# Performance work log

Hardware: AMD Instinct MI355X
Metric: run time of the kernel (lower is better)

The kernel has to match this reference:

```python
import jax, jax.numpy as jnp
import numpy as np

N, E, F_IN, HEADS, OUT_PER_HEAD = 50000, 1600000, 128, 4, 32
NEG_SLOPE = 0.2  # LeakyReLU slope used by standard GATConv


def setup_inputs() -> dict:
    key = jax.random.key(0)
    ks = jax.random.split(key, 7)
    x = jax.random.normal(ks[0], (N, F_IN), dtype=jnp.float32)
    edge_src = jax.random.randint(ks[1], (E,), 0, N, dtype=jnp.int64)
    edge_dst = jax.random.randint(ks[2], (E,), 0, N, dtype=jnp.int64)
    W = jax.random.normal(ks[3], (F_IN, HEADS * OUT_PER_HEAD), dtype=jnp.float32) / np.float32(np.sqrt(F_IN))
    a_src = jax.random.normal(ks[4], (HEADS, OUT_PER_HEAD), dtype=jnp.float32) * 0.1
    a_dst = jax.random.normal(ks[5], (HEADS, OUT_PER_HEAD), dtype=jnp.float32) * 0.1
    bias = jnp.zeros((HEADS * OUT_PER_HEAD,), dtype=jnp.float32)
    return {"x": x, "W": W, "a_src": a_src, "a_dst": a_dst, "bias": bias,
            "edge_src": edge_src, "edge_dst": edge_dst}


def reference(x, W, a_src, a_dst, bias, edge_src, edge_dst):
    # GATConv with concat=True over a static edge list (the faithful
    # static-shape form of tf.where(adj>0.5) -> gather -> GAT -> scatter).
    n = x.shape[0]
    H, D = a_src.shape
    h = (x @ W).reshape(n, H, D)                      # [N,H,D] projected features
    # per-node attention logits for source / destination roles
    e_s = jnp.einsum('nhd,hd->nh', h, a_src)          # [N,H]
    e_d = jnp.einsum('nhd,hd->nh', h, a_dst)          # [N,H]
    # per-edge logits with LeakyReLU
    e = jax.nn.leaky_relu(e_s[edge_src] + e_d[edge_dst], NEG_SLOPE)  # [E,H]
    # numerically stable softmax over incoming edges of each destination node
    m = jax.ops.segment_max(e, edge_dst, num_segments=n)             # [N,H]
    m = jnp.where(jnp.isfinite(m), m, 0.0)
    alpha = jnp.exp(e - m[edge_dst])                                 # [E,H]
    denom = jax.ops.segment_sum(alpha, edge_dst, num_segments=n)     # [N,H]
    alpha = alpha / jnp.where(denom > 0, denom, 1.0)[edge_dst]
    # weighted aggregation of source features onto destinations
    msgs = alpha[:, :, None] * h[edge_src]                           # [E,H,D]
    out = jax.ops.segment_sum(msgs, edge_dst, num_segments=n)        # [N,H,D]
    return out.reshape(n, H * D) + bias
```

## Files before the change

### kernel.cpp

```cpp
#include <hip/hip_runtime.h>
#include <math.h>

#define NEG_SLOPE 0.2f
#define XROW 136
#define BSHIFT 4
#define BNODES 16
#define NBUCK_MAX 3200
#define CAP 768
#define CPAD 32
#define NSB 256
#define STASH 6272

typedef __attribute__((ext_vector_type(8))) short short8;
typedef __attribute__((ext_vector_type(4))) float floatx4;

__device__ __forceinline__ unsigned short f2bf(float f) {
    unsigned int u = __float_as_uint(f);
    u += 0x7fffu + ((u >> 16) & 1u);
    return (unsigned short)(u >> 16);
}
__device__ __forceinline__ float bf2f(unsigned short b) {
    return __uint_as_float(((unsigned int)b) << 16);
}
__device__ __forceinline__ float u2fl(unsigned int u) {
    return __uint_as_float(u << 16);
}
__device__ __forceinline__ float u2fh(unsigned int u) {
    return __uint_as_float(u & 0xffff0000u);
}

__device__ __forceinline__ void fma8(float* a, int o, float wt, const uint4& hv) {
    a[o + 0] = fmaf(wt, u2fl(hv.x), a[o + 0]);
    a[o + 1] = fmaf(wt, u2fh(hv.x), a[o + 1]);
    a[o + 2] = fmaf(wt, u2fl(hv.y), a[o + 2]);
    a[o + 3] = fmaf(wt, u2fh(hv.y), a[o + 3]);
    a[o + 4] = fmaf(wt, u2fl(hv.z), a[o + 4]);
    a[o + 5] = fmaf(wt, u2fh(hv.z), a[o + 5]);
    a[o + 6] = fmaf(wt, u2fl(hv.w), a[o + 6]);
    a[o + 7] = fmaf(wt, u2fh(hv.w), a[o + 7]);
}

__global__ __launch_bounds__(256) void prep_w_kernel(
    const float* __restrict__ W, unsigned short* __restrict__ WThi,
    unsigned short* __restrict__ WTlo, int* __restrict__ gcur, int nbuck)
{
    const int idx = blockIdx.x * 256 + threadIdx.x;
    const int j = idx >> 7, k = idx & 127;
    const float w = W[k * 128 + j];
    const unsigned short hi = f2bf(w);
    WThi[idx] = hi;
    WTlo[idx] = f2bf(w - bf2f(hi));
    if (idx < nbuck) gcur[idx * CPAD] = idx * CAP;
}

__global__ __launch_bounds__(1024) void scatter_kernel(
    const int* __restrict__ src, const int* __restrict__ dst,
    int* __restrict__ gcur, int* __restrict__ ebuf, int e, int nbuck)
{
    __shared__ unsigned int stash[STASH];
    __shared__ int cnt[NBUCK_MAX];
    const int t = threadIdx.x;
    for (int b = t; b < nbuck; b += 1024) cnt[b] = 0;
    __syncthreads();
    const int eph = (((e + NSB - 1) / NSB) + 3) & ~3;
    const int base = blockIdx.x * eph;
    const int m = min(e - base, eph);
    if (m > 0) {
        const int m4 = m >> 2;
        for (int j = t; j < m4; j += 1024) {
            const int i0 = base + j * 4;
            const int4 s4 = *(const int4*)(src + i0);
            const int4 d4 = *(const int4*)(dst + i0);
            stash[j * 4 + 0] = (unsigned)s4.x | ((unsigned)(d4.x & 15) << 16)
                             | ((unsigned)(d4.x >> BSHIFT) << 20);
            atomicAdd(&cnt[d4.x >> BSHIFT], 1);
            stash[j * 4 + 1] = (unsigned)s4.y | ((unsigned)(d4.y & 15) << 16)
                             | ((unsigned)(d4.y >> BSHIFT) << 20);
            atomicAdd(&cnt[d4.y >> BSHIFT], 1);
            stash[j * 4 + 2] = (unsigned)s4.z | ((unsigned)(d4.z & 15) << 16)
                             | ((unsigned)(d4.z >> BSHIFT) << 20);
            atomicAdd(&cnt[d4.z >> BSHIFT], 1);
            stash[j * 4 + 3] = (unsigned)s4.w | ((unsigned)(d4.w & 15) << 16)
                             | ((unsigned)(d4.w >> BSHIFT) << 20);
            atomicAdd(&cnt[d4.w >> BSHIFT], 1);
        }
        for (int j = m4 * 4 + t; j < m; j += 1024) {
            const int d = dst[base + j];
            stash[j] = (unsigned)src[base + j] | ((unsigned)(d & 15) << 16)
                     | ((unsigned)(d >> BSHIFT) << 20);
            atomicAdd(&cnt[d >> BSHIFT], 1);
        }
    }
    __syncthreads();
    for (int b = t; b < nbuck; b += 1024) {
        const int c = cnt[b];
        if (c > 0) cnt[b] = atomicAdd(&gcur[b * CPAD], c);
    }
    __syncthreads();
    for (int j = t; j < m; j += 1024) {
        const unsigned int v = stash[j];
        const int bk = v >> 20;
        const int pos = atomicAdd(&cnt[bk], 1);
        if (pos < bk * CAP + CAP) ebuf[pos] = (int)(v & 0xFFFFFu);
    }
}

__global__ __launch_bounds__(256, 2) void mfma_gemm_kernel(
    const float* __restrict__ x, const unsigned short* __restrict__ WThi,
    const unsigned short* __restrict__ WTlo, const float* __restrict__ a_src,
    const float* __restrict__ a_dst, unsigned short* __restrict__ hb,
    float* __restrict__ es, float* __restrict__ ed, int n)
{
    __shared__ unsigned short Xhi[32 * XROW];
    __shared__ unsigned short Xlo[32 * XROW];
    const int t = threadIdx.x;
    const int wv = t >> 6, lane = t & 63;
    const int l16 = lane & 15, quad = lane >> 4;
    const int node_base = blockIdx.x * 32;

    float4 xv[4];
    #pragma unroll
    for (int it = 0; it < 4; ++it) {
        const int i = t + it * 256;
        const int nd = i >> 5, k4 = i & 31;
        float4 v = make_float4(0.f, 0.f, 0.f, 0.f);
        if (node_base + nd < n)
            v = ((const float4*)(x + (size_t)(node_base + nd) * 128))[k4];
        xv[it] = v;
    }
    #pragma unroll
    for (int it = 0; it < 4; ++it) {
        const int i = t + it * 256;
        const int nd = i >> 5, k4 = i & 31;
        const float4 v = xv[it];
        const unsigned short h0 = f2bf(v.x), h1 = f2bf(v.y),
                             h2 = f2bf(v.z), h3 = f2bf(v.w);
        const unsigned short l0 = f2bf(v.x - bf2f(h0)), l1 = f2bf(v.y - bf2f(h1)),
                             l2 = f2bf(v.z - bf2f(h2)), l3 = f2bf(v.w - bf2f(h3));
        *(ushort4*)&Xhi[nd * XROW + k4 * 4] = make_ushort4(h0, h1, h2, h3);
        *(ushort4*)&Xlo[nd * XROW + k4 * 4] = make_ushort4(l0, l1, l2, l3);
    }

    short8 bh[4][2], bl[4][2];
    #pragma unroll
    for (int c = 0; c < 4; ++c) {
        #pragma unroll
        for (int u = 0; u < 2; ++u) {
            const int j = (wv * 2 + u) * 16 + l16;
            const int ko = c * 32 + quad * 8;
            bh[c][u] = *(const short8*)&WThi[j * 128 + ko];
            bl[c][u] = *(const short8*)&WTlo[j * 128 + ko];
        }
    }
    __syncthreads();

    floatx4 acc[2][2] = {};
    #pragma unroll
    for (int c = 0; c < 4; ++c) {
        const int ko = c * 32 + quad * 8;
        short8 ah[2], al[2];
        #pragma unroll
        for (int r = 0; r < 2; ++r) {
            ah[r] = *(const short8*)&Xhi[(r * 16 + l16) * XROW + ko];
            al[r] = *(const short8*)&Xlo[(r * 16 + l16) * XROW + ko];
        }
        #pragma unroll
        for (int r = 0; r < 2; ++r)
        #pragma unroll
        for (int u = 0; u < 2; ++u) {
            acc[r][u] = __builtin_amdgcn_mfma_f32_16x16x32_bf16(ah[r], bl[c][u], acc[r][u], 0, 0, 0);
            acc[r][u] = __builtin_amdgcn_mfma_f32_16x16x32_bf16(al[r], bh[c][u], acc[r][u], 0, 0, 0);
            acc[r][u] = __builtin_amdgcn_mfma_f32_16x16x32_bf16(ah[r], bh[c][u], acc[r][u], 0, 0, 0);
        }
    }

    float asv[2], adv[2];
    #pragma unroll
    for (int u = 0; u < 2; ++u) {
        const int feat = (wv * 2 + u) * 16 + l16;
        asv[u] = a_src[feat];
        adv[u] = a_dst[feat];
    }
    #pragma unroll
    for (int r = 0; r < 2; ++r) {
        #pragma unroll
        for (int u = 0; u < 2; ++u) {
            const int feat = (wv * 2 + u) * 16 + l16;
            #pragma unroll
            for (int g = 0; g < 4; ++g) {
                const int node = node_base + r * 16 + quad * 4 + g;
                if (node < n)
                    hb[(size_t)node * 128 + feat] = f2bf(acc[r][u][g]);
            }
        }
        #pragma unroll
        for (int g = 0; g < 4; ++g) {
            float ps = acc[r][0][g] * asv[0] + acc[r][1][g] * asv[1];
            float pd = acc[r][0][g] * adv[0] + acc[r][1][g] * adv[1];
            #pragma unroll
            for (int o = 8; o >= 1; o >>= 1) {
                ps += __shfl_xor(ps, o);
                pd += __shfl_xor(pd, o);
            }
            const int node = node_base + r * 16 + quad * 4 + g;
            if (l16 == 0 && node < n) {
                es[node * 4 + wv] = ps;
                ed[node * 4 + wv] = pd;
            }
        }
    }
}

__global__ __launch_bounds__(256) void sort_agg_kernel(
    const unsigned short* __restrict__ hb, const float* __restrict__ es,
    const float* __restrict__ ed, const float* __restrict__ bias,
    const int* __restrict__ gcur, const int* __restrict__ ebuf,
    float* __restrict__ out, int n)
{
    __shared__ unsigned short esort[CAP];
    __shared__ int hist[BNODES], hexcl[BNODES], cur[BNODES];
    const int b = blockIdx.x;
    const int t = threadIdx.x;
    const int lane = t & 63;
    const int wv = t >> 6;
    const int l8 = lane & 7;
    const int oct = lane >> 3;
    const int f0 = l8 * 16;
    const int hh = l8 >> 1;

    const int start = b * CAP;
    const int end = start + min(gcur[b * CPAD] - start, CAP);

    if (t < BNODES) hist[t] = 0;
    __syncthreads();
    for (int i = start + t; i < end; i += 256)
        atomicAdd(&hist[(ebuf[i] >> 16) & (BNODES - 1)], 1);
    __syncthreads();
    if (wv == 0) {
        const int v = (lane < BNODES) ? hist[lane] : 0;
        int incl = v;
        #pragma unroll
        for (int o = 1; o < BNODES; o <<= 1) {
            const int tt = __shfl_up(incl, o);
            if (lane >= o) incl += tt;
        }
        if (lane < BNODES) { hexcl[lane] = incl - v; cur[lane] = incl - v; }
    }
    __syncthreads();
    for (int i = start + t; i < end; i += 256) {
        const int v = ebuf[i];
        const int pos = atomicAdd(&cur[(v >> 16) & (BNODES - 1)], 1);
        if (pos < CAP) esort[pos] = (unsigned short)(v & 0xFFFF);
    }
    __syncthreads();

    for (int j = 0; j < 4; ++j) {
        const int nd = wv * 4 + j;
        const int node = b * BNODES + nd;
        if (node >= n) break;
        const int off = hexcl[nd];
        const int deg = hist[nd];
        const float edh = ed[(size_t)node * 4 + hh];

        float a[16];
        #pragma unroll
        for (int k = 0; k < 16; ++k) a[k] = 0.f;
        float wsum = 0.f;

        for (int c0 = 0; c0 < deg; c0 += 16) {
            const int ci0 = c0 + oct;
            const int ci1 = ci0 + 8;
            const int dm = deg - 1;
            const int s0 = esort[min(off + min(ci0, dm), CAP - 1)];
            const int s1 = esort[min(off + min(ci1, dm), CAP - 1)];
            const float e0 = es[(size_t)s0 * 4 + hh];
            const float e1 = es[(size_t)s1 * 4 + hh];
            const uint4 hA0 = *(const uint4*)&hb[(size_t)s0 * 128 + f0];
            const uint4 hB0 = *(const uint4*)&hb[(size_t)s0 * 128 + f0 + 8];
            const uint4 hA1 = *(const uint4*)&hb[(size_t)s1 * 128 + f0];
            const uint4 hB1 = *(const uint4*)&hb[(size_t)s1 * 128 + f0 + 8];
            float lg0 = e0 + edh; lg0 = lg0 > 0.f ? lg0 : NEG_SLOPE * lg0;
            float lg1 = e1 + edh; lg1 = lg1 > 0.f ? lg1 : NEG_SLOPE * lg1;
            const float w0 = (ci0 < deg) ? __expf(lg0) : 0.f;
            const float w1 = (ci1 < deg) ? __expf(lg1) : 0.f;
            fma8(a, 0, w0, hA0); fma8(a, 8, w0, hB0);
            fma8(a, 0, w1, hA1); fma8(a, 8, w1, hB1);
            wsum += w0 + w1;
        }
        #pragma unroll
        for (int o = 8; o <= 32; o <<= 1) {
            #pragma unroll
            for (int k = 0; k < 16; ++k) a[k] += __shfl_xor(a[k], o);
            wsum += __shfl_xor(wsum, o);
        }
        if (oct == 0) {
            const float inv = 1.f / ((wsum > 0.f) ? wsum : 1.f);
            #pragma unroll
            for (int q = 0; q < 4; ++q) {
                const float4 bq = *(const float4*)(bias + f0 + q * 4);
                float4 o4;
                o4.x = a[q * 4 + 0] * inv + bq.x;
                o4.y = a[q * 4 + 1] * inv + bq.y;
                o4.z = a[q * 4 + 2] * inv + bq.z;
                o4.w = a[q * 4 + 3] * inv + bq.w;
                *(float4*)(out + (size_t)node * 128 + f0 + q * 4) = o4;
            }
        }
    }
}

extern "C" void kernel_launch(void* const* d_in, const int* in_sizes, int n_in,
                              void* d_out, int out_size, void* d_ws, size_t ws_size,
                              hipStream_t stream)
{
    const float* x      = (const float*)d_in[0];
    const float* W      = (const float*)d_in[1];
    const float* a_src  = (const float*)d_in[2];
    const float* a_dst  = (const float*)d_in[3];
    const float* bias   = (const float*)d_in[4];
    const int*   e_src  = (const int*)d_in[5];
    const int*   e_dst  = (const int*)d_in[6];
    float* out = (float*)d_out;

    const int n = in_sizes[0] / 128;
    const int e = in_sizes[5];
    const int nbuck = (n + BNODES - 1) >> BSHIFT;

    char* ws = (char*)d_ws;
    size_t o = 0;
    auto alloc = [&](size_t bytes) { void* p = ws + o; o += (bytes + 255) & ~(size_t)255; return p; };
    unsigned short* hb   = (unsigned short*)alloc((size_t)n * 128 * sizeof(unsigned short));
    unsigned short* WThi = (unsigned short*)alloc(128 * 128 * sizeof(unsigned short));
    unsigned short* WTlo = (unsigned short*)alloc(128 * 128 * sizeof(unsigned short));
    float* es      = (float*)alloc((size_t)n * 4 * sizeof(float));
    float* ed      = (float*)alloc((size_t)n * 4 * sizeof(float));
    int* gcur      = (int*)alloc((size_t)nbuck * CPAD * sizeof(int));
    int* ebuf      = (int*)alloc((size_t)nbuck * CAP * sizeof(int));
    (void)ws_size; (void)n_in; (void)out_size;

    prep_w_kernel<<<64, 256, 0, stream>>>(W, WThi, WTlo, gcur, nbuck);
    scatter_kernel<<<NSB, 1024, 0, stream>>>(e_src, e_dst, gcur, ebuf, e, nbuck);
    mfma_gemm_kernel<<<(n + 31) / 32, 256, 0, stream>>>(x, WThi, WTlo, a_src, a_dst,
                                                        hb, es, ed, n);
    sort_agg_kernel<<<nbuck, 256, 0, stream>>>(hb, es, ed, bias, gcur, ebuf, out, n);
}
```

Measured before the change: 215.0 us.

## Widen dst buckets to 64-node regions, stage GEMM output through LDS

Destination buckets grow from 16 to 64 nodes (about 800 regions instead of 3200), and the aggregation kernel moves to 512 threads per block. This cuts the number of global cursor atomics and the per-block histogram overhead, and the per-block flush of cursors now starts at a rotated offset to spread contention. The GEMM kernel loads B fragments per output column group to lower register pressure and raises launch bounds to 4 blocks per SM. It also transposes bf16 results through shared memory so h rows are written with coalesced 16-byte stores. Fixed per-region capacity (RCAP) can drop edges if a region's in-degree is skewed, and there are fewer, larger aggregation blocks.

```diff
diff --git a/kernel.cpp b/kernel.cpp
--- a/kernel.cpp
+++ b/kernel.cpp
@@ -3,10 +3,10 @@
 
 #define NEG_SLOPE 0.2f
 #define XROW 136
-#define BSHIFT 4
-#define BNODES 16
-#define NBUCK_MAX 3200
-#define CAP 768
+#define RSHIFT 6
+#define RNODES 64
+#define NREG_MAX 800
+#define RCAP 2432
 #define CPAD 32
 #define NSB 256
 #define STASH 6272
@@ -42,7 +42,7 @@
 
 __global__ __launch_bounds__(256) void prep_w_kernel(
     const float* __restrict__ W, unsigned short* __restrict__ WThi,
-    unsigned short* __restrict__ WTlo, int* __restrict__ gcur, int nbuck)
+    unsigned short* __restrict__ WTlo, int* __restrict__ gcur, int nreg)
 {
     const int idx = blockIdx.x * 256 + threadIdx.x;
     const int j = idx >> 7, k = idx & 127;
@@ -50,17 +50,17 @@
     const unsigned short hi = f2bf(w);
     WThi[idx] = hi;
     WTlo[idx] = f2bf(w - bf2f(hi));
-    if (idx < nbuck) gcur[idx * CPAD] = idx * CAP;
+    if (idx < nreg) gcur[idx * CPAD] = idx * RCAP;
 }
 
 __global__ __launch_bounds__(1024) void scatter_kernel(
     const int* __restrict__ src, const int* __restrict__ dst,
-    int* __restrict__ gcur, int* __restrict__ ebuf, int e, int nbuck)
+    int* __restrict__ gcur, int* __restrict__ ebuf, int e, int nreg)
 {
     __shared__ unsigned int stash[STASH];
-    __shared__ int cnt[NBUCK_MAX];
+    __shared__ int cnt[NREG_MAX];
     const int t = threadIdx.x;
-    for (int b = t; b < nbuck; b += 1024) cnt[b] = 0;
+    for (int b = t; b < nreg; b += 1024) cnt[b] = 0;
     __syncthreads();
     const int eph = (((e + NSB - 1) / NSB) + 3) & ~3;
     const int base = blockIdx.x * eph;
@@ -71,41 +71,46 @@
             const int i0 = base + j * 4;
             const int4 s4 = *(const int4*)(src + i0);
             const int4 d4 = *(const int4*)(dst + i0);
-            stash[j * 4 + 0] = (unsigned)s4.x | ((unsigned)(d4.x & 15) << 16)
-                             | ((unsigned)(d4.x >> BSHIFT) << 20);
-            atomicAdd(&cnt[d4.x >> BSHIFT], 1);
-            stash[j * 4 + 1] = (unsigned)s4.y | ((unsigned)(d4.y & 15) << 16)
-                             | ((unsigned)(d4.y >> BSHIFT) << 20);
-            atomicAdd(&cnt[d4.y >> BSHIFT], 1);
-            stash[j * 4 + 2] = (unsigned)s4.z | ((unsigned)(d4.z & 15) << 16)
-                             | ((unsigned)(d4.z >> BSHIFT) << 20);
-            atomicAdd(&cnt[d4.z >> BSHIFT], 1);
-            stash[j * 4 + 3] = (unsigned)s4.w | ((unsigned)(d4.w & 15) << 16)
-                             | ((unsigned)(d4.w >> BSHIFT) << 20);
-            atomicAdd(&cnt[d4.w >> BSHIFT], 1);
+            stash[j * 4 + 0] = (unsigned)s4.x | ((unsigned)(d4.x & 63) << 16)
+                             | ((unsigned)(d4.x >> RSHIFT) << 22);
+            atomicAdd(&cnt[d4.x >> RSHIFT], 1);
+            stash[j * 4 + 1] = (unsigned)s4.y | ((unsigned)(d4.y & 63) << 16)
+                             | ((unsigned)(d4.y >> RSHIFT) << 22);
+            atomicAdd(&cnt[d4.y >> RSHIFT], 1);
+            stash[j * 4 + 2] = (unsigned)s4.z | ((unsigned)(d4.z & 63) << 16)
+                             | ((unsigned)(d4.z >> RSHIFT) << 22);
+            atomicAdd(&cnt[d4.z >> RSHIFT], 1);
+            stash[j * 4 + 3] = (unsigned)s4.w | ((unsigned)(d4.w & 63) << 16)
+                             | ((unsigned)(d4.w >> RSHIFT) << 22);
+            atomicAdd(&cnt[d4.w >> RSHIFT], 1);
         }
         for (int j = m4 * 4 + t; j < m; j += 1024) {
             const int d = dst[base + j];
-            stash[j] = (unsigned)src[base + j] | ((unsigned)(d & 15) << 16)
-                     | ((unsigned)(d >> BSHIFT) << 20);
-            atomicAdd(&cnt[d >> BSHIFT], 1);
-        }
-    }
-    __syncthreads();
-    for (int b = t; b < nbuck; b += 1024) {
-        const int c = cnt[b];
-        if (c > 0) cnt[b] = atomicAdd(&gcur[b * CPAD], c);
+            stash[j] = (unsigned)src[base + j] | ((unsigned)(d & 63) << 16)
+                     | ((unsigned)(d >> RSHIFT) << 22);
+            atomicAdd(&cnt[d >> RSHIFT], 1);
+        }
+    }
+    __syncthreads();
+    {
+        const int off0 = (blockIdx.x * 97) % nreg;
+        for (int i = t; i < nreg; i += 1024) {
+            int b = i + off0;
+            if (b >= nreg) b -= nreg;
+            const int c = cnt[b];
+            if (c > 0) cnt[b] = atomicAdd(&gcur[b * CPAD], c);
+        }
     }
     __syncthreads();
     for (int j = t; j < m; j += 1024) {
         const unsigned int v = stash[j];
-        const int bk = v >> 20;
+        const int bk = v >> 22;
         const int pos = atomicAdd(&cnt[bk], 1);
-        if (pos < bk * CAP + CAP) ebuf[pos] = (int)(v & 0xFFFFFu);
-    }
-}
-
-__global__ __launch_bounds__(256, 2) void mfma_gemm_kernel(
+        if (pos < bk * RCAP + RCAP) ebuf[pos] = (int)(v & 0x3FFFFFu);
+    }
+}
+
+__global__ __launch_bounds__(256, 4) void mfma_gemm_kernel(
     const float* __restrict__ x, const unsigned short* __restrict__ WThi,
     const unsigned short* __restrict__ WTlo, const float* __restrict__ a_src,
     const float* __restrict__ a_dst, unsigned short* __restrict__ hb,
@@ -140,37 +145,30 @@
         *(ushort4*)&Xhi[nd * XROW + k4 * 4] = make_ushort4(h0, h1, h2, h3);
         *(ushort4*)&Xlo[nd * XROW + k4 * 4] = make_ushort4(l0, l1, l2, l3);
     }
-
-    short8 bh[4][2], bl[4][2];
-    #pragma unroll
-    for (int c = 0; c < 4; ++c) {
-        #pragma unroll
-        for (int u = 0; u < 2; ++u) {
-            const int j = (wv * 2 + u) * 16 + l16;
+    __syncthreads();
+
+    floatx4 acc[2][2] = {};
+    #pragma unroll
+    for (int u = 0; u < 2; ++u) {
+        short8 bh[4], bl[4];
+        const int j = (wv * 2 + u) * 16 + l16;
+        #pragma unroll
+        for (int c = 0; c < 4; ++c) {
             const int ko = c * 32 + quad * 8;
-            bh[c][u] = *(const short8*)&WThi[j * 128 + ko];
-            bl[c][u] = *(const short8*)&WTlo[j * 128 + ko];
-        }
-    }
-    __syncthreads();
-
-    floatx4 acc[2][2] = {};
-    #pragma unroll
-    for (int c = 0; c < 4; ++c) {
-        const int ko = c * 32 + quad * 8;
-        short8 ah[2], al[2];
-        #pragma unroll
-        for (int r = 0; r < 2; ++r) {
-            ah[r] = *(const short8*)&Xhi[(r * 16 + l16) * XROW + ko];
-            al[r] = *(const short8*)&Xlo[(r * 16 + l16) * XROW + ko];
-        }
-        #pragma unroll
-        for (int r = 0; r < 2; ++r)
-        #pragma unroll
-        for (int u = 0; u < 2; ++u) {
-            acc[r][u] = __builtin_amdgcn_mfma_f32_16x16x32_bf16(ah[r], bl[c][u], acc[r][u], 0, 0, 0);
-            acc[r][u] = __builtin_amdgcn_mfma_f32_16x16x32_bf16(al[r], bh[c][u], acc[r][u], 0, 0, 0);
-            acc[r][u] = __builtin_amdgcn_mfma_f32_16x16x32_bf16(ah[r], bh[c][u], acc[r][u], 0, 0, 0);
+            bh[c] = *(const short8*)&WThi[j * 128 + ko];
+            bl[c] = *(const short8*)&WTlo[j * 128 + ko];
+        }
+        #pragma unroll
+        for (int c = 0; c < 4; ++c) {
+            const int ko = c * 32 + quad * 8;
+            #pragma unroll
+            for (int r = 0; r < 2; ++r) {
+                const short8 ah = *(const short8*)&Xhi[(r * 16 + l16) * XROW + ko];
+                const short8 al = *(const short8*)&Xlo[(r * 16 + l16) * XROW + ko];
+                acc[r][u] = __builtin_amdgcn_mfma_f32_16x16x32_bf16(ah, bl[c], acc[r][u], 0, 0, 0);
+                acc[r][u] = __builtin_amdgcn_mfma_f32_16x16x32_bf16(al, bh[c], acc[r][u], 0, 0, 0);
+                acc[r][u] = __builtin_amdgcn_mfma_f32_16x16x32_bf16(ah, bh[c], acc[r][u], 0, 0, 0);
+            }
         }
     }
 
@@ -183,16 +181,6 @@
     }
     #pragma unroll
     for (int r = 0; r < 2; ++r) {
-        #pragma unroll
-        for (int u = 0; u < 2; ++u) {
-            const int feat = (wv * 2 + u) * 16 + l16;
-            #pragma unroll
-            for (int g = 0; g < 4; ++g) {
-                const int node = node_base + r * 16 + quad * 4 + g;
-                if (node < n)
-                    hb[(size_t)node * 128 + feat] = f2bf(acc[r][u][g]);
-            }
-        }
         #pragma unroll
         for (int g = 0; g < 4; ++g) {
             float ps = acc[r][0][g] * asv[0] + acc[r][1][g] * asv[1];
@@ -209,16 +197,39 @@
             }
         }
     }
-}
-
-__global__ __launch_bounds__(256) void sort_agg_kernel(
+
+    __syncthreads();
+    unsigned short* T = Xhi;
+    #pragma unroll
+    for (int r = 0; r < 2; ++r)
+    #pragma unroll
+    for (int u = 0; u < 2; ++u) {
+        const int feat = (wv * 2 + u) * 16 + l16;
+        #pragma unroll
+        for (int g = 0; g < 4; ++g)
+            T[(r * 16 + quad * 4 + g) * 128 + feat] = f2bf(acc[r][u][g]);
+    }
+    __syncthreads();
+    {
+        const int row = t >> 3, seg = t & 7;
+        const int node = node_base + row;
+        if (node < n) {
+            const uint4 v0 = *(const uint4*)&T[row * 128 + seg * 16];
+            const uint4 v1 = *(const uint4*)&T[row * 128 + seg * 16 + 8];
+            *(uint4*)&hb[(size_t)node * 128 + seg * 16] = v0;
+            *(uint4*)&hb[(size_t)node * 128 + seg * 16 + 8] = v1;
+        }
+    }
+}
+
+__global__ __launch_bounds__(512) void sort_agg_kernel(
     const unsigned short* __restrict__ hb, const float* __restrict__ es,
     const float* __restrict__ ed, const float* __restrict__ bias,
     const int* __restrict__ gcur, const int* __restrict__ ebuf,
     float* __restrict__ out, int n)
 {
-    __shared__ unsigned short esort[CAP];
-    __shared__ int hist[BNODES], hexcl[BNODES], cur[BNODES];
+    __shared__ unsigned short esort[RCAP];
+    __shared__ int hist[RNODES], hexcl[RNODES], cur[RNODES];
     const int b = blockIdx.x;
     const int t = threadIdx.x;
     const int lane = t & 63;
@@ -228,35 +239,36 @@
     const int f0 = l8 * 16;
     const int hh = l8 >> 1;
 
-    const int start = b * CAP;
-    const int end = start + min(gcur[b * CPAD] - start, CAP);
-
-    if (t < BNODES) hist[t] = 0;
-    __syncthreads();
-    for (int i = start + t; i < end; i += 256)
-        atomicAdd(&hist[(ebuf[i] >> 16) & (BNODES - 1)], 1);
+    const int start = b * RCAP;
+    const int end = start + min(gcur[b * CPAD] - start, RCAP);
+
+    if (t < RNODES) hist[t] = 0;
+    __syncthreads();
+    for (int i = start + t; i < end; i += 512)
+        atomicAdd(&hist[(ebuf[i] >> 16) & (RNODES - 1)], 1);
     __syncthreads();
     if (wv == 0) {
-        const int v = (lane < BNODES) ? hist[lane] : 0;
+        const int v = hist[lane];
         int incl = v;
         #pragma unroll
-        for (int o = 1; o < BNODES; o <<= 1) {
+        for (int o = 1; o < RNODES; o <<= 1) {
             const int tt = __shfl_up(incl, o);
             if (lane >= o) incl += tt;
         }
-        if (lane < BNODES) { hexcl[lane] = incl - v; cur[lane] = incl - v; }
-    }
-    __syncthreads();
-    for (int i = start + t; i < end; i += 256) {
+        hexcl[lane] = incl - v;
+        cur[lane] = incl - v;
+    }
+    __syncthreads();
+    for (int i = start + t; i < end; i += 512) {
         const int v = ebuf[i];
-        const int pos = atomicAdd(&cur[(v >> 16) & (BNODES - 1)], 1);
-        if (pos < CAP) esort[pos] = (unsigned short)(v & 0xFFFF);
-    }
-    __syncthreads();
-
-    for (int j = 0; j < 4; ++j) {
-        const int nd = wv * 4 + j;
-        const int node = b * BNODES + nd;
+        const int pos = atomicAdd(&cur[(v >> 16) & (RNODES - 1)], 1);
+        if (pos < RCAP) esort[pos] = (unsigned short)(v & 0xFFFF);
+    }
+    __syncthreads();
+
+    for (int j = 0; j < 8; ++j) {
+        const int nd = wv * 8 + j;
+        const int node = b * RNODES + nd;
         if (node >= n) break;
         const int off = hexcl[nd];
         const int deg = hist[nd];
@@ -271,8 +283,8 @@
             const int ci0 = c0 + oct;
             const int ci1 = ci0 + 8;
             const int dm = deg - 1;
-            const int s0 = esort[min(off + min(ci0, dm), CAP - 1)];
-            const int s1 = esort[min(off + min(ci1, dm), CAP - 1)];
+            const int s0 = esort[min(off + min(ci0, dm), RCAP - 1)];
+            const int s1 = esort[min(off + min(ci1, dm), RCAP - 1)];
             const float e0 = es[(size_t)s0 * 4 + hh];
             const float e1 = es[(size_t)s1 * 4 + hh];
             const uint4 hA0 = *(const uint4*)&hb[(size_t)s0 * 128 + f0];
@@ -324,7 +336,7 @@
 
     const int n = in_sizes[0] / 128;
     const int e = in_sizes[5];
-    const int nbuck = (n + BNODES - 1) >> BSHIFT;
+    const int nreg = (n + RNODES - 1) >> RSHIFT;
 
     char* ws = (char*)d_ws;
     size_t o = 0;
@@ -334,13 +346,13 @@
     unsigned short* WTlo = (unsigned short*)alloc(128 * 128 * sizeof(unsigned short));
     float* es      = (float*)alloc((size_t)n * 4 * sizeof(float));
     float* ed      = (float*)alloc((size_t)n * 4 * sizeof(float));
-    int* gcur      = (int*)alloc((size_t)nbuck * CPAD * sizeof(int));
-    int* ebuf      = (int*)alloc((size_t)nbuck * CAP * sizeof(int));
+    int* gcur      = (int*)alloc((size_t)nreg * CPAD * sizeof(int));
+    int* ebuf      = (int*)alloc((size_t)nreg * RCAP * sizeof(int));
     (void)ws_size; (void)n_in; (void)out_size;
 
-    prep_w_kernel<<<64, 256, 0, stream>>>(W, WThi, WTlo, gcur, nbuck);
-    scatter_kernel<<<NSB, 1024, 0, stream>>>(e_src, e_dst, gcur, ebuf, e, nbuck);
+    prep_w_kernel<<<64, 256, 0, stream>>>(W, WThi, WTlo, gcur, nreg);
+    scatter_kernel<<<NSB, 1024, 0, stream>>>(e_src, e_dst, gcur, ebuf, e, nreg);
     mfma_gemm_kernel<<<(n + 31) / 32, 256, 0, stream>>>(x, WThi, WTlo, a_src, a_dst,
                                                         hb, es, ed, n);
-    sort_agg_kernel<<<nbuck, 256, 0, stream>>>(hb, es, ed, bias, gcur, ebuf, out, n);
-}
+    sort_agg_kernel<<<nreg, 512, 0, stream>>>(hb, es, ed, bias, gcur, ebuf, out, n);
+}
```

Result: faster. 198.2 us (-7.8%).
